# Kernel tuning notes

Measured on AMD Instinct MI355X. Metric: run time of the kernel, lower is better.

The kernel has to match this reference:

```python
import jax, jax.numpy as jnp
import numpy as np

POS_THR = 0.5
NEG_THR = 0.4
WEIGHTS = (1.0, 1.0, 1.0, 1.0)


def _box_iou(a, b):
    # a: (N,4), b: (M,4) in xyxy -> (N,M) IoU
    area_a = (a[:, 2] - a[:, 0]) * (a[:, 3] - a[:, 1])  # (N,)
    area_b = (b[:, 2] - b[:, 0]) * (b[:, 3] - b[:, 1])  # (M,)
    lt = jnp.maximum(a[:, None, :2], b[None, :, :2])  # (N,M,2)
    rb = jnp.minimum(a[:, None, 2:], b[None, :, 2:])  # (N,M,2)
    wh = jnp.clip(rb - lt, 0.0)
    inter = wh[..., 0] * wh[..., 1]  # (N,M)
    return inter / (area_a[:, None] + area_b[None, :] - inter)


def _encode(anchors, gt):
    # both (N,4) xyxy -> (N,4) deltas (dx,dy,dw,dh)
    eps = jnp.finfo(jnp.float32).eps
    ax = (anchors[:, 0] + anchors[:, 2]) * 0.5
    ay = (anchors[:, 1] + anchors[:, 3]) * 0.5
    aw = jnp.maximum(anchors[:, 2] - anchors[:, 0], eps)
    ah = jnp.maximum(anchors[:, 3] - anchors[:, 1], eps)
    gx = (gt[:, 0] + gt[:, 2]) * 0.5
    gy = (gt[:, 1] + gt[:, 3]) * 0.5
    gw = gt[:, 2] - gt[:, 0]
    gh = gt[:, 3] - gt[:, 1]
    dx = (gx - ax) / aw
    dy = (gy - ay) / ah
    dw = jnp.log(gw / aw)
    dh = jnp.log(gh / ah)
    w = jnp.asarray(WEIGHTS, dtype=jnp.float32)
    return jnp.stack((dx, dy, dw, dh), axis=-1) * w


def setup_inputs() -> dict:
    key = jax.random.key(0)
    k1, k2, k3, k4, k5 = jax.random.split(key, 5)
    N, M, IMG = 200000, 128, 1024.0
    # valid anchor boxes: random centers + sizes in [8, 512]
    ac = jax.random.uniform(k1, (N, 2), dtype=jnp.float32) * IMG
    asz = 8.0 + jax.random.uniform(k2, (N, 2), dtype=jnp.float32) * 504.0
    anchors = jnp.concatenate([ac - 0.5 * asz, ac + 0.5 * asz], axis=-1)
    gc = jax.random.uniform(k3, (M, 2), dtype=jnp.float32) * IMG
    gsz = 16.0 + jax.random.uniform(k4, (M, 2), dtype=jnp.float32) * 480.0
    gt_boxes = jnp.concatenate([gc - 0.5 * gsz, gc + 0.5 * gsz], axis=-1)
    gt_labels = jax.random.randint(k5, (M,), 1, 81, dtype=jnp.int64 if jax.config.jax_enable_x64 else jnp.int32)
    return {"anchors": anchors, "gt_boxes": gt_boxes, "gt_labels": gt_labels}


def reference(anchors, gt_boxes, gt_labels):
    iou = _box_iou(anchors, gt_boxes)  # (N,M)
    max_iou_per_anchor = iou.max(axis=1)              # (N,)
    matched_gt_idx = iou.argmax(axis=1)               # (N,)
    matched_anchor_per_gt = iou.argmax(axis=0)        # (M,)
    pos_mask = max_iou_per_anchor >= POS_THR
    pos_mask = pos_mask.at[matched_anchor_per_gt].set(True)  # force best anchor per gt positive
    neg_mask = (max_iou_per_anchor < NEG_THR) & (~pos_mask)
    cls_targets = jnp.where(pos_mask, gt_labels[matched_gt_idx].astype(jnp.int32),
                            jnp.where(neg_mask, 0, -1))
    enc = _encode(anchors, gt_boxes[matched_gt_idx])  # (N,4)
    reg_targets = jnp.where(pos_mask[:, None], enc, 0.0)
    return cls_targets, reg_targets, pos_mask
```

## Files before the change

kernel.cpp:

```cpp
#include <hip/hip_runtime.h>
#include <cmath>
#include <cstdint>

#pragma clang fp contract(off)

typedef unsigned long long ull;

constexpr float POS_THR = 0.5f;
constexpr float NEG_THR = 0.4f;
constexpr float F32_EPS = 1.1920928955078125e-07f;

__device__ __forceinline__ float area_of(const float4 b) {
    return __fmul_rn(__fsub_rn(b.z, b.x), __fsub_rn(b.w, b.y));
}

__device__ __forceinline__ float iou_one(const float4 a, const float area_a,
                                         const float4 g, const float area_g) {
    float lx = fmaxf(a.x, g.x);
    float ly = fmaxf(a.y, g.y);
    float rx = fminf(a.z, g.z);
    float ry = fminf(a.w, g.w);
    float w  = fmaxf(__fsub_rn(rx, lx), 0.0f);
    float h  = fmaxf(__fsub_rn(ry, ly), 0.0f);
    float inter = __fmul_rn(w, h);
    float denom = __fsub_rn(__fadd_rn(area_a, area_g), inter);
    return __fdiv_rn(inter, denom);
}

__device__ __forceinline__ float4 encode_box(const float4 a, const float4 g) {
    float ax = (a.x + a.z) * 0.5f;
    float ay = (a.y + a.w) * 0.5f;
    float aw = fmaxf(a.z - a.x, F32_EPS);
    float ah = fmaxf(a.w - a.y, F32_EPS);
    float gx = (g.x + g.z) * 0.5f;
    float gy = (g.y + g.w) * 0.5f;
    float gw = g.z - g.x;
    float gh = g.w - g.y;
    return make_float4((gx - ax) / aw, (gy - ay) / ah, logf(gw / aw), logf(gh / ah));
}

__device__ __forceinline__ ull shfl_xor_u64(ull key, int off) {
    unsigned lo = (unsigned)key;
    unsigned hi = (unsigned)(key >> 32);
    lo = __shfl_xor(lo, off, 64);
    hi = __shfl_xor(hi, off, 64);
    return ((ull)hi << 32) | lo;
}

__global__ __launch_bounds__(256, 4) void fused_kernel(
    const float4* __restrict__ anchors, const float4* __restrict__ gts,
    const int* __restrict__ labels, int n, int m, int nblocks,
    float* __restrict__ out_cls, float4* __restrict__ out_reg,
    float* __restrict__ out_pos, ull* __restrict__ ws)
{
    __shared__ float4         sA[128];
    __shared__ unsigned       sKv[128][17];
    __shared__ unsigned short sKi[128][17];
    __shared__ unsigned       sCv[128][17];

    const int t = threadIdx.x;
    const int base = blockIdx.x * 128;

    if (t < 128) {
        int i = base + t;
        float4 a = make_float4(0.0f, 0.0f, 0.0f, 0.0f);
        if (i < n) a = anchors[i];
        sA[t] = a;
    }

    const int tx = t & 15;
    const int ty = t >> 4;
    const int g0 = tx * 8;
    const int a0 = ty * 8;

    float4 g[8];
    float  ga[8];
    #pragma unroll
    for (int j = 0; j < 8; ++j) {
        g[j]  = gts[g0 + j];
        ga[j] = area_of(g[j]);
    }

    float cbest[8];
    #pragma unroll
    for (int j = 0; j < 8; ++j) cbest[j] = -1.0f;

    __syncthreads();

    #pragma unroll
    for (int ap = 0; ap < 4; ++ap) {
        const int ai0 = 2 * ap, ai1 = 2 * ap + 1;
        float4 aA = sA[a0 + ai0];
        float4 aB = sA[a0 + ai1];
        float aaA = area_of(aA);
        float aaB = area_of(aB);
        float rbA = -1.0f, rbB = -1.0f;
        int   rjA = 0,     rjB = 0;
        #pragma unroll
        for (int j = 0; j < 8; ++j) {
            float v0 = iou_one(aA, aaA, g[j], ga[j]);
            float v1 = iou_one(aB, aaB, g[j], ga[j]);
            if (v0 > rbA) { rbA = v0; rjA = j; }
            if (v1 > rbB) { rbB = v1; rjB = j; }
            cbest[j] = fmaxf(cbest[j], fmaxf(v0, v1));
        }
        sKv[a0 + ai0][tx] = __float_as_uint(rbA);
        sKi[a0 + ai0][tx] = (unsigned short)(g0 + rjA);
        sKv[a0 + ai1][tx] = __float_as_uint(rbB);
        sKi[a0 + ai1][tx] = (unsigned short)(g0 + rjB);
    }
    #pragma unroll
    for (int j = 0; j < 8; ++j)
        sCv[g0 + j][ty] = __float_as_uint(cbest[j]);

    __syncthreads();

    if (t < 128) {
        unsigned bv = sKv[t][0];
        unsigned bi = sKi[t][0];
        #pragma unroll
        for (int x = 1; x < 16; ++x) {
            unsigned v  = sKv[t][x];
            unsigned ii = sKi[t][x];
            if (v > bv || (v == bv && ii < bi)) { bv = v; bi = ii; }
        }
        int i = base + t;
        if (i < n) {
            float best = __uint_as_float(bv);
            int bestj  = (int)bi;
            bool pos = best >= POS_THR;
            bool neg = (best < NEG_THR) && !pos;
            out_cls[i] = pos ? (float)labels[bestj] : (neg ? 0.0f : -1.0f);
            out_pos[i] = pos ? 1.0f : 0.0f;
            float4 enc = make_float4(0.0f, 0.0f, 0.0f, 0.0f);
            if (pos) enc = encode_box(sA[t], gts[bestj]);
            out_reg[i] = enc;
        }
    } else {
        int j = t - 128;
        unsigned bv = sCv[j][0];
        #pragma unroll
        for (int y = 1; y < 16; ++y) { unsigned v = sCv[j][y]; if (v > bv) bv = v; }
        ws[(size_t)j * nblocks + blockIdx.x] =
            ((ull)bv << 32) | (ull)(~(unsigned)blockIdx.x);
    }
}

__global__ __launch_bounds__(128) void reduce_fixup(
    const float4* __restrict__ anchors, const float4* __restrict__ gts,
    const int* __restrict__ labels, int n, int m, int nblocks,
    float* __restrict__ out_cls, float4* __restrict__ out_reg,
    float* __restrict__ out_pos, const ull* __restrict__ ws)
{
    __shared__ ull redu[2];
    __shared__ ull s_akey;
    __shared__ ull s_bkey;
    __shared__ ull s_ckey;

    const int j = blockIdx.x;
    const int t = threadIdx.x;
    const ull* wj = ws + (size_t)j * nblocks;

    ull key = 0ull;
    for (int b = t; b < nblocks; b += 128) { ull k = wj[b]; if (k > key) key = k; }
    #pragma unroll
    for (int off = 32; off > 0; off >>= 1) {
        ull o = shfl_xor_u64(key, off);
        if (o > key) key = o;
    }
    if ((t & 63) == 0) redu[t >> 6] = key;
    __syncthreads();
    if (t == 0) s_akey = redu[0] > redu[1] ? redu[0] : redu[1];
    __syncthreads();
    const unsigned B = ~(unsigned)s_akey;

    float4 gj = gts[j];
    float gaj = area_of(gj);
    {
        int i = (int)B * 128 + t;
        float4 a = make_float4(0.0f, 0.0f, 0.0f, 0.0f);
        if (i < n) a = anchors[i];
        float aa = area_of(a);
        float v = iou_one(a, aa, gj, gaj);
        ull kb = ((ull)__float_as_uint(v) << 32) | (ull)(~(unsigned)t);
        #pragma unroll
        for (int off = 32; off > 0; off >>= 1) {
            ull o = shfl_xor_u64(kb, off);
            if (o > kb) kb = o;
        }
        __syncthreads();
        if ((t & 63) == 0) redu[t >> 6] = kb;
    }
    __syncthreads();
    if (t == 0) s_bkey = redu[0] > redu[1] ? redu[0] : redu[1];
    __syncthreads();
    const int giW = (int)B * 128 + (int)(~(unsigned)s_bkey);

    float4 aw = anchors[giW];
    float aaw = area_of(aw);
    ull k2 = 0ull;
    if (t < m) {
        float4 gt_t = gts[t];
        float gat = area_of(gt_t);
        float v2 = iou_one(aw, aaw, gt_t, gat);
        k2 = ((ull)__float_as_uint(v2) << 32) | (ull)(~(unsigned)t);
    }
    #pragma unroll
    for (int off = 32; off > 0; off >>= 1) {
        ull o = shfl_xor_u64(k2, off);
        if (o > k2) k2 = o;
    }
    __syncthreads();
    if ((t & 63) == 0) redu[t >> 6] = k2;
    __syncthreads();
    if (t == 0) {
        s_ckey = redu[0] > redu[1] ? redu[0] : redu[1];
        int bj = (int)(~(unsigned)s_ckey);
        out_pos[giW] = 1.0f;
        out_cls[giW] = (float)labels[bj];
        out_reg[giW] = encode_box(aw, gts[bj]);
    }
}

extern "C" void kernel_launch(void* const* d_in, const int* in_sizes, int n_in,
                              void* d_out, int out_size, void* d_ws, size_t ws_size,
                              hipStream_t stream)
{
    const float4* anchors = (const float4*)d_in[0];
    const float4* gts     = (const float4*)d_in[1];
    const int*    labels  = (const int*)d_in[2];
    int n = in_sizes[0] / 4;
    int m = in_sizes[1] / 4;

    float*  out     = (float*)d_out;
    float*  out_cls = out;
    float4* out_reg = (float4*)(out + n);
    float*  out_pos = out + 5 * (size_t)n;
    ull*    ws      = (ull*)d_ws;

    int nblocks = (n + 127) / 128;
    fused_kernel<<<nblocks, 256, 0, stream>>>(anchors, gts, labels, n, m, nblocks,
                                              out_cls, out_reg, out_pos, ws);
    reduce_fixup<<<m, 128, 0, stream>>>(anchors, gts, labels, n, m, nblocks,
                                        out_cls, out_reg, out_pos, ws);
}
```

Before: 92.94 us.

## Process two anchor tiles per block to halve per-gt partial workspace

Each block of the fused kernel now loops over two 128-anchor tiles, reusing the gt boxes and areas held in registers and combining the per-gt column maxima across both tiles before writing a single workspace entry. This halves the grid size and the number of per-gt partial keys the fixup kernel has to scan. The fixup kernel moves to 256 threads to match the 256-anchor block granularity. The cost is extra barriers per block and less parallelism from the smaller grid. The gt index stored in shared memory shrinks to a byte, which assumes m is at most 256.

Result: slower. 96.15 us (+3.5%).

```diff
diff --git a/kernel.cpp b/kernel.cpp
--- a/kernel.cpp
+++ b/kernel.cpp
@@ -53,21 +53,12 @@
     float* __restrict__ out_cls, float4* __restrict__ out_reg,
     float* __restrict__ out_pos, ull* __restrict__ ws)
 {
-    __shared__ float4         sA[128];
-    __shared__ unsigned       sKv[128][17];
-    __shared__ unsigned short sKi[128][17];
-    __shared__ unsigned       sCv[128][17];
+    __shared__ float4        sA[128];
+    __shared__ unsigned      sRv[128][17];
+    __shared__ unsigned char sRi[128][17];
+    __shared__ unsigned      sCv[128][17];
 
     const int t = threadIdx.x;
-    const int base = blockIdx.x * 128;
-
-    if (t < 128) {
-        int i = base + t;
-        float4 a = make_float4(0.0f, 0.0f, 0.0f, 0.0f);
-        if (i < n) a = anchors[i];
-        sA[t] = a;
-    }
-
     const int tx = t & 15;
     const int ty = t >> 4;
     const int g0 = tx * 8;
@@ -81,88 +72,105 @@
         ga[j] = area_of(g[j]);
     }
 
-    float cbest[8];
-    #pragma unroll
-    for (int j = 0; j < 8; ++j) cbest[j] = -1.0f;
-
-    __syncthreads();
-
-    #pragma unroll
-    for (int ap = 0; ap < 4; ++ap) {
-        const int ai0 = 2 * ap, ai1 = 2 * ap + 1;
-        float4 aA = sA[a0 + ai0];
-        float4 aB = sA[a0 + ai1];
-        float aaA = area_of(aA);
-        float aaB = area_of(aB);
-        float rbA = -1.0f, rbB = -1.0f;
-        int   rjA = 0,     rjB = 0;
-        #pragma unroll
-        for (int j = 0; j < 8; ++j) {
-            float v0 = iou_one(aA, aaA, g[j], ga[j]);
-            float v1 = iou_one(aB, aaB, g[j], ga[j]);
-            if (v0 > rbA) { rbA = v0; rjA = j; }
-            if (v1 > rbB) { rbB = v1; rjB = j; }
-            cbest[j] = fmaxf(cbest[j], fmaxf(v0, v1));
-        }
-        sKv[a0 + ai0][tx] = __float_as_uint(rbA);
-        sKi[a0 + ai0][tx] = (unsigned short)(g0 + rjA);
-        sKv[a0 + ai1][tx] = __float_as_uint(rbB);
-        sKi[a0 + ai1][tx] = (unsigned short)(g0 + rjB);
-    }
-    #pragma unroll
-    for (int j = 0; j < 8; ++j)
-        sCv[g0 + j][ty] = __float_as_uint(cbest[j]);
-
-    __syncthreads();
-
-    if (t < 128) {
-        unsigned bv = sKv[t][0];
-        unsigned bi = sKi[t][0];
-        #pragma unroll
-        for (int x = 1; x < 16; ++x) {
-            unsigned v  = sKv[t][x];
-            unsigned ii = sKi[t][x];
-            if (v > bv || (v == bv && ii < bi)) { bv = v; bi = ii; }
-        }
-        int i = base + t;
-        if (i < n) {
-            float best = __uint_as_float(bv);
-            int bestj  = (int)bi;
-            bool pos = best >= POS_THR;
-            bool neg = (best < NEG_THR) && !pos;
-            out_cls[i] = pos ? (float)labels[bestj] : (neg ? 0.0f : -1.0f);
-            out_pos[i] = pos ? 1.0f : 0.0f;
-            float4 enc = make_float4(0.0f, 0.0f, 0.0f, 0.0f);
-            if (pos) enc = encode_box(sA[t], gts[bestj]);
-            out_reg[i] = enc;
-        }
-    } else {
+    unsigned cbv = 0u;
+
+    for (int tile = 0; tile < 2; ++tile) {
+        const int base = blockIdx.x * 256 + tile * 128;
+
+        if (t < 128) {
+            int i = base + t;
+            float4 a = make_float4(0.0f, 0.0f, 0.0f, 0.0f);
+            if (i < n) a = anchors[i];
+            sA[t] = a;
+        }
+        __syncthreads();
+
+        float cb[8];
+        #pragma unroll
+        for (int j = 0; j < 8; ++j) cb[j] = -1.0f;
+
+        #pragma unroll
+        for (int ap = 0; ap < 4; ++ap) {
+            const int ai0 = 2 * ap, ai1 = 2 * ap + 1;
+            float4 aA = sA[a0 + ai0];
+            float4 aB = sA[a0 + ai1];
+            float aaA = area_of(aA);
+            float aaB = area_of(aB);
+            float rbA = -1.0f, rbB = -1.0f;
+            int   rjA = 0,     rjB = 0;
+            #pragma unroll
+            for (int j = 0; j < 8; ++j) {
+                float v0 = iou_one(aA, aaA, g[j], ga[j]);
+                float v1 = iou_one(aB, aaB, g[j], ga[j]);
+                if (v0 > rbA) { rbA = v0; rjA = j; }
+                if (v1 > rbB) { rbB = v1; rjB = j; }
+                cb[j] = fmaxf(cb[j], fmaxf(v0, v1));
+            }
+            sRv[a0 + ai0][tx] = __float_as_uint(rbA);
+            sRi[a0 + ai0][tx] = (unsigned char)(g0 + rjA);
+            sRv[a0 + ai1][tx] = __float_as_uint(rbB);
+            sRi[a0 + ai1][tx] = (unsigned char)(g0 + rjB);
+        }
+        #pragma unroll
+        for (int j = 0; j < 8; ++j)
+            sCv[g0 + j][ty] = __float_as_uint(cb[j]);
+
+        __syncthreads();
+
+        if (t < 128) {
+            unsigned bv = sRv[t][0];
+            unsigned bi = sRi[t][0];
+            #pragma unroll
+            for (int x = 1; x < 16; ++x) {
+                unsigned v  = sRv[t][x];
+                unsigned ii = sRi[t][x];
+                if (v > bv || (v == bv && ii < bi)) { bv = v; bi = ii; }
+            }
+            int i = base + t;
+            if (i < n) {
+                float best = __uint_as_float(bv);
+                int bestj  = (int)bi;
+                bool pos = best >= POS_THR;
+                bool neg = (best < NEG_THR) && !pos;
+                out_cls[i] = pos ? (float)labels[bestj] : (neg ? 0.0f : -1.0f);
+                out_pos[i] = pos ? 1.0f : 0.0f;
+                float4 enc = make_float4(0.0f, 0.0f, 0.0f, 0.0f);
+                if (pos) enc = encode_box(sA[t], gts[bestj]);
+                out_reg[i] = enc;
+            }
+        } else {
+            int j = t - 128;
+            unsigned bv = sCv[j][0];
+            #pragma unroll
+            for (int y = 1; y < 16; ++y) { unsigned v = sCv[j][y]; if (v > bv) bv = v; }
+            if (bv > cbv) cbv = bv;
+        }
+        __syncthreads();
+    }
+
+    if (t >= 128) {
         int j = t - 128;
-        unsigned bv = sCv[j][0];
-        #pragma unroll
-        for (int y = 1; y < 16; ++y) { unsigned v = sCv[j][y]; if (v > bv) bv = v; }
         ws[(size_t)j * nblocks + blockIdx.x] =
-            ((ull)bv << 32) | (ull)(~(unsigned)blockIdx.x);
-    }
-}
-
-__global__ __launch_bounds__(128) void reduce_fixup(
+            ((ull)cbv << 32) | (ull)(~(unsigned)blockIdx.x);
+    }
+}
+
+__global__ __launch_bounds__(256) void reduce_fixup(
     const float4* __restrict__ anchors, const float4* __restrict__ gts,
     const int* __restrict__ labels, int n, int m, int nblocks,
     float* __restrict__ out_cls, float4* __restrict__ out_reg,
     float* __restrict__ out_pos, const ull* __restrict__ ws)
 {
-    __shared__ ull redu[2];
+    __shared__ ull redu[4];
     __shared__ ull s_akey;
     __shared__ ull s_bkey;
-    __shared__ ull s_ckey;
 
     const int j = blockIdx.x;
     const int t = threadIdx.x;
     const ull* wj = ws + (size_t)j * nblocks;
 
     ull key = 0ull;
-    for (int b = t; b < nblocks; b += 128) { ull k = wj[b]; if (k > key) key = k; }
+    for (int b = t; b < nblocks; b += 256) { ull k = wj[b]; if (k > key) key = k; }
     #pragma unroll
     for (int off = 32; off > 0; off >>= 1) {
         ull o = shfl_xor_u64(key, off);
@@ -170,14 +178,19 @@
     }
     if ((t & 63) == 0) redu[t >> 6] = key;
     __syncthreads();
-    if (t == 0) s_akey = redu[0] > redu[1] ? redu[0] : redu[1];
+    if (t == 0) {
+        ull k = redu[0];
+        #pragma unroll
+        for (int w2 = 1; w2 < 4; ++w2) if (redu[w2] > k) k = redu[w2];
+        s_akey = k;
+    }
     __syncthreads();
     const unsigned B = ~(unsigned)s_akey;
 
     float4 gj = gts[j];
     float gaj = area_of(gj);
     {
-        int i = (int)B * 128 + t;
+        int i = (int)B * 256 + t;
         float4 a = make_float4(0.0f, 0.0f, 0.0f, 0.0f);
         if (i < n) a = anchors[i];
         float aa = area_of(a);
@@ -192,9 +205,14 @@
         if ((t & 63) == 0) redu[t >> 6] = kb;
     }
     __syncthreads();
-    if (t == 0) s_bkey = redu[0] > redu[1] ? redu[0] : redu[1];
-    __syncthreads();
-    const int giW = (int)B * 128 + (int)(~(unsigned)s_bkey);
+    if (t == 0) {
+        ull k = redu[0];
+        #pragma unroll
+        for (int w2 = 1; w2 < 4; ++w2) if (redu[w2] > k) k = redu[w2];
+        s_bkey = k;
+    }
+    __syncthreads();
+    const int giW = (int)B * 256 + (int)(~(unsigned)s_bkey);
 
     float4 aw = anchors[giW];
     float aaw = area_of(aw);
@@ -214,8 +232,10 @@
     if ((t & 63) == 0) redu[t >> 6] = k2;
     __syncthreads();
     if (t == 0) {
-        s_ckey = redu[0] > redu[1] ? redu[0] : redu[1];
-        int bj = (int)(~(unsigned)s_ckey);
+        ull kk = redu[0];
+        #pragma unroll
+        for (int w2 = 1; w2 < 4; ++w2) if (redu[w2] > kk) kk = redu[w2];
+        int bj = (int)(~(unsigned)kk);
         out_pos[giW] = 1.0f;
         out_cls[giW] = (float)labels[bj];
         out_reg[giW] = encode_box(aw, gts[bj]);
@@ -238,9 +258,9 @@
     float*  out_pos = out + 5 * (size_t)n;
     ull*    ws      = (ull*)d_ws;
 
-    int nblocks = (n + 127) / 128;
+    int nblocks = (n + 255) / 256;
     fused_kernel<<<nblocks, 256, 0, stream>>>(anchors, gts, labels, n, m, nblocks,
                                               out_cls, out_reg, out_pos, ws);
-    reduce_fixup<<<m, 128, 0, stream>>>(anchors, gts, labels, n, m, nblocks,
+    reduce_fixup<<<m, 256, 0, stream>>>(anchors, gts, labels, n, m, nblocks,
                                         out_cls, out_reg, out_pos, ws);
 }
```
